# Performance work log

Hardware: AMD Instinct MI355X
Metric: run time of the kernel (lower is better)

The kernel has to match this reference:

```python
import jax, jax.numpy as jnp
import numpy as np

B, N, FIN, H, D = 8, 2048, 64, 4, 32
ALPHA = 0.2  # LeakyReLU negative slope


def setup_inputs() -> dict:
    key = jax.random.key(0)
    k1, k2, k3, k4 = jax.random.split(key, 4)
    h = jax.random.normal(k1, (B, N, FIN), dtype=jnp.float32)
    adj = jax.random.randint(k2, (B, N, N), 0, 2).astype(jnp.int32)
    # ensure self-loops so every softmax row has at least one unmasked entry
    idx = jnp.arange(N)
    adj = adj.at[:, idx, idx].set(1)
    W = jax.random.normal(k3, (FIN, H * D), dtype=jnp.float32) * 0.1
    a = jax.random.normal(k4, (H, 2 * D), dtype=jnp.float32) * 0.1
    return {"h": h, "adj": adj, "W": W, "a": a}


def reference(h, adj, W, a):
    # h: (B,N,Fin), adj: (B,N,N) int, W: (Fin,H*D), a: (H,2D)
    Bn, Nn, _ = h.shape
    Hh, twoD = a.shape
    Dd = twoD // 2
    Wh = (h @ W).reshape(Bn, Nn, Hh, Dd).transpose(0, 2, 1, 3)  # (B,H,N,D)
    # e_ij = leakyrelu(Wh_i . a1 + Wh_j . a2) -- avoids O(N^2 * 2D) concat
    src = jnp.einsum('bhnd,hd->bhn', Wh, a[:, :Dd])  # (B,H,N)
    dst = jnp.einsum('bhnd,hd->bhn', Wh, a[:, Dd:])  # (B,H,N)
    e = jax.nn.leaky_relu(src[:, :, :, None] + dst[:, :, None, :], negative_slope=ALPHA)  # (B,H,N,N)
    e = jnp.where(adj[:, None, :, :] == 0, -jnp.inf, e)
    attn = jax.nn.softmax(e, axis=-1)  # (B,H,N,N)
    out = jnp.einsum('bhij,bhjd->bhid', attn, Wh)  # (B,H,N,D)
    return out.transpose(0, 2, 1, 3).reshape(Bn, Nn, Hh * Dd)
```

## Files before the change

kernel.cpp:

```cpp
#include <hip/hip_runtime.h>

typedef short short8 __attribute__((ext_vector_type(8)));
typedef _Float16 half8 __attribute__((ext_vector_type(8)));
typedef _Float16 half2v __attribute__((ext_vector_type(2)));
typedef float floatx4 __attribute__((ext_vector_type(4)));

extern "C" __device__ _Float16 __ocml_exp2_f16(_Float16);

#define B_   8
#define N_   2048
#define FIN_ 64
#define H_   4
#define D_   32
#define HD_  128
#define JH_  1024
#define ALPHA_ 0.2f
#define LOG2E_ 1.4426950408889634f


__global__ __launch_bounds__(256) void gat_prep4(
    const float* __restrict__ h, const float* __restrict__ W, const float* __restrict__ a,
    unsigned short* __restrict__ WhF, float* __restrict__ src, unsigned short* __restrict__ dstb)
{
    __shared__ float Ws[FIN_][HD_];
    __shared__ float hsT[FIN_][36];
    int bx = blockIdx.x;
    int b = bx >> 6;
    int n0 = (bx & 63) * 32;
    int tid = threadIdx.x;

    #pragma unroll
    for (int it = 0; it < 8; ++it) {
        int idx = it * 256 + tid;
        int k = idx >> 5, c4 = (idx & 31) << 2;
        *(float4*)&Ws[k][c4] = *(const float4*)&W[k * HD_ + c4];
    }
    #pragma unroll
    for (int it = 0; it < 8; ++it) {
        int idx = it * 256 + tid;
        int r = idx >> 6, k = idx & 63;
        hsT[k][r] = h[((size_t)b * N_ + n0 + r) * FIN_ + k];
    }
    __syncthreads();

    int c = tid & 127;
    int rq = tid >> 7;
    int hh = c >> 5, d = c & 31;
    float acc[16];
    #pragma unroll
    for (int r = 0; r < 16; ++r) acc[r] = 0.f;
    for (int k = 0; k < FIN_; ++k) {
        float wv = Ws[k][c];
        float4 h0 = *(const float4*)&hsT[k][rq * 16];
        float4 h1 = *(const float4*)&hsT[k][rq * 16 + 4];
        float4 h2 = *(const float4*)&hsT[k][rq * 16 + 8];
        float4 h3 = *(const float4*)&hsT[k][rq * 16 + 12];
        acc[0]  += h0.x * wv; acc[1]  += h0.y * wv; acc[2]  += h0.z * wv; acc[3]  += h0.w * wv;
        acc[4]  += h1.x * wv; acc[5]  += h1.y * wv; acc[6]  += h1.z * wv; acc[7]  += h1.w * wv;
        acc[8]  += h2.x * wv; acc[9]  += h2.y * wv; acc[10] += h2.z * wv; acc[11] += h2.w * wv;
        acc[12] += h3.x * wv; acc[13] += h3.y * wv; acc[14] += h3.z * wv; acc[15] += h3.w * wv;
    }

    {
        int half = d >> 4, n = d & 15;
        int j0 = n0 + rq * 16;
        int it0 = j0 >> 5;
        int g0 = (j0 >> 3) & 3;
        #pragma unroll
        for (int rr = 0; rr < 2; ++rr) {
            __attribute__((aligned(16))) unsigned pk4[4];
            #pragma unroll
            for (int q = 0; q < 4; ++q)
                pk4[q] = __builtin_bit_cast(unsigned,
                    __builtin_amdgcn_cvt_pkrtz(acc[rr * 8 + 2 * q], acc[rr * 8 + 2 * q + 1]));
            size_t fi = ((((size_t)b * H_ + hh) * 64 + it0) * 2 + half) * 64
                        + (size_t)(g0 + rr) * 16 + n;
            *(uint4*)&WhF[fi * 8] = *(uint4*)pk4;
        }
    }

    float a1v = a[hh * 64 + d];
    float a2v = a[hh * 64 + 32 + d];
    #pragma unroll
    for (int r = 0; r < 16; ++r) {
        float s1 = acc[r] * a1v;
        float s2 = acc[r] * a2v;
        #pragma unroll
        for (int off = 16; off >= 1; off >>= 1) {
            s1 += __shfl_xor(s1, off, 32);
            s2 += __shfl_xor(s2, off, 32);
        }
        if (d == 0) {
            int n = n0 + rq * 16 + r;
            src[(b * H_ + hh) * N_ + n] = s1 * LOG2E_;
            _Float16 hv = (_Float16)(s2 * LOG2E_);
            dstb[(b * H_ + hh) * N_ + n] = __builtin_bit_cast(unsigned short, hv);
        }
    }
}

__global__ __launch_bounds__(256, 4) void gat_main11(
    const int* __restrict__ adj, const unsigned short* __restrict__ WhF,
    const float* __restrict__ src, const unsigned short* __restrict__ dstb,
    float* __restrict__ pO, float* __restrict__ pW)
{
    __shared__ unsigned short dsts[H_ * JH_];
    __shared__ unsigned adjW[16][36];

    int bx = blockIdx.x;
    int b    = bx >> 8;
    int rest = bx & 255;
    int half = rest & 1;
    int i0   = (rest >> 1) * 16;
    int jb   = half * JH_;
    int tid = threadIdx.x;
    int wv = tid >> 6, l = tid & 63;

    #pragma unroll
    for (int it = 0; it < 2; ++it) {
        int idx = it * 256 + tid;
        int hh = idx >> 7, off = (idx & 127) * 8;
        *(uint4*)&dsts[hh * JH_ + off] =
            *(const uint4*)&dstb[(size_t)(b * H_ + hh) * N_ + jb + off];
    }

    const int* adjBase = adj + ((size_t)(b * N_ + i0 + wv * 4)) * N_ + jb + l;

    int vals[16];
    #pragma unroll
    for (int rr = 0; rr < 4; ++rr)
        #pragma unroll
        for (int cc = 0; cc < 4; ++cc)
            vals[rr * 4 + cc] = adjBase[rr * N_ + cc * 64];

    int h = wv, g = l >> 4, m = l & 15;
    int g8 = g << 3;
    _Float16 sv = (_Float16)src[(b * H_ + h) * N_ + i0 + m];
    half2v s2; s2[0] = sv; s2[1] = sv;
    const _Float16 alf = (_Float16)0.2f;
    const unsigned short* WhB =
        WhF + (((size_t)(b * H_ + h) * 64 + half * 32)) * 1024 + l * 8;
    const unsigned short* dstH = &dsts[h * JH_];

    short8 onesS;
    #pragma unroll
    for (int q = 0; q < 8; ++q) onesS[q] = (short)0x3C00;
    half8 ones = __builtin_bit_cast(half8, onesS);

    floatx4 acc0 = {0.f, 0.f, 0.f, 0.f};
    floatx4 acc1 = {0.f, 0.f, 0.f, 0.f};
    floatx4 acc2 = {0.f, 0.f, 0.f, 0.f};

    short8 bf0_c = *(const short8*)&WhB[0];
    short8 bf1_c = *(const short8*)&WhB[512];
    uint4 dv_c;

    for (int q = 0; q < 4; ++q) {
        #pragma unroll
        for (int rr = 0; rr < 4; ++rr)
            #pragma unroll
            for (int cc = 0; cc < 4; ++cc) {
                unsigned long long mk = __ballot(vals[rr * 4 + cc] != 0);
                if (l == 0) {
                    int c = q * 4 + cc;
                    adjW[wv * 4 + rr][2 * c]     = (unsigned)mk;
                    adjW[wv * 4 + rr][2 * c + 1] = (unsigned)(mk >> 32);
                }
            }
        __syncthreads();
        if (q == 0) dv_c = *(const uint4*)&dstH[g8];

        if (q < 3) {
            #pragma unroll
            for (int rr = 0; rr < 4; ++rr)
                #pragma unroll
                for (int cc = 0; cc < 4; ++cc)
                    vals[rr * 4 + cc] = adjBase[rr * N_ + (q + 1) * 256 + cc * 64];
        }

        for (int jj = 0; jj < 8; ++jj) {
            int it = q * 8 + jj;
            int fn = (it + 1) * 1024;
            short8 bf0_n = *(const short8*)&WhB[fn];
            short8 bf1_n = *(const short8*)&WhB[fn + 512];
            int j0n = ((it + 1) << 5) + g8;
            uint4  dv_n  = *(const uint4*)&dstH[(j0n < JH_) ? j0n : g8];

            unsigned sh = adjW[m][it] >> g8;
            const unsigned* du = (const unsigned*)&dv_c;
            __attribute__((aligned(16))) unsigned pk[4];
            #pragma unroll
            for (int c2 = 0; c2 < 4; ++c2) {
                half2v d2 = __builtin_bit_cast(half2v, du[c2]);
                half2v e2 = s2 + d2;
                half2v t2 = e2 * alf;
                e2 = __builtin_elementwise_max(e2, t2);
                half2v x2;
                x2[0] = __ocml_exp2_f16(e2[0]);
                x2[1] = __ocml_exp2_f16(e2[1]);
                unsigned mk = ((((sh >> (2 * c2 + 1)) & 1u) << 16)
                               | ((sh >> (2 * c2)) & 1u)) * 0x3C00u;
                x2 = x2 * __builtin_bit_cast(half2v, mk);
                pk[c2] = __builtin_bit_cast(unsigned, x2);
            }
            half8 af = __builtin_bit_cast(half8, *(uint4*)pk);
            acc0 = __builtin_amdgcn_mfma_f32_16x16x32_f16(
                       af, __builtin_bit_cast(half8, bf0_c), acc0, 0, 0, 0);
            acc1 = __builtin_amdgcn_mfma_f32_16x16x32_f16(
                       af, __builtin_bit_cast(half8, bf1_c), acc1, 0, 0, 0);
            acc2 = __builtin_amdgcn_mfma_f32_16x16x32_f16(af, ones, acc2, 0, 0, 0);
            bf0_c = bf0_n; bf1_c = bf1_n; dv_c = dv_n;
        }
    }

    if (m == 0) {
        #pragma unroll
        for (int r = 0; r < 4; ++r)
            pW[(((size_t)half * B_ + b) * H_ + h) * N_ + i0 + g * 4 + r] = acc2[r];
    }
    #pragma unroll
    for (int r = 0; r < 4; ++r) {
        size_t o = ((size_t)(half * B_ + b) * N_ + i0 + g * 4 + r) * HD_ + h * 32 + m;
        pO[o]      = acc0[r];
        pO[o + 16] = acc1[r];
    }
}

__global__ __launch_bounds__(256) void gat_fin(
    const float* __restrict__ pO, const float* __restrict__ pW, float* __restrict__ out)
{
    int gid = blockIdx.x * 256 + threadIdx.x;
    int c4 = (gid & 31) << 2;
    int i  = (gid >> 5) & (N_ - 1);
    int b  = gid >> 16;
    int hh = c4 >> 5;
    float w0 = pW[((size_t)b * H_ + hh) * N_ + i];
    float w1 = pW[(((size_t)B_ + b) * H_ + hh) * N_ + i];
    float inv = 1.f / (w0 + w1);
    size_t o = ((size_t)b * N_ + i) * HD_ + c4;
    float4 v0 = *(const float4*)&pO[o];
    float4 v1 = *(const float4*)&pO[(size_t)B_ * N_ * HD_ + o];
    float4 r;
    r.x = (v0.x + v1.x) * inv;
    r.y = (v0.y + v1.y) * inv;
    r.z = (v0.z + v1.z) * inv;
    r.w = (v0.w + v1.w) * inv;
    *(float4*)&out[o] = r;
}

extern "C" void kernel_launch(void* const* d_in, const int* in_sizes, int n_in,
                              void* d_out, int out_size, void* d_ws, size_t ws_size,
                              hipStream_t stream) {
    const float* h   = (const float*)d_in[0];
    const int*   adj = (const int*)d_in[1];
    const float* W   = (const float*)d_in[2];
    const float* a   = (const float*)d_in[3];
    float* out = (float*)d_out;

    unsigned short* WhF  = (unsigned short*)d_ws;
    float*          src  = (float*)((char*)d_ws + 4u * 1024 * 1024);
    unsigned short* dstb = (unsigned short*)((char*)d_ws + 4u * 1024 * 1024 + 256u * 1024);
    float*          pO   = (float*)((char*)d_ws + 8u * 1024 * 1024);
    float*          pW   = (float*)((char*)d_ws + 24u * 1024 * 1024);

    gat_prep4<<<B_ * (N_ / 32), 256, 0, stream>>>(h, W, a, WhF, src, dstb);
    gat_main11<<<B_ * (N_ / 16) * 2, 256, 0, stream>>>(adj, WhF, src, dstb, pO, pW);
    gat_fin<<<(B_ * N_ * HD_ / 4) / 256, 256, 0, stream>>>(pO, pW, out);
}
```

Before: 230.7 us.

## Drop the split over neighbour columns and normalize inside the main kernel

Each block now processes all 2048 neighbour columns for its 16 rows instead of half of them. This removes the partial-sum buffers and the separate finalize kernel, so softmax normalization happens directly in registers before the output is written. The change removes one launch and the round trip of partial outputs through global memory. In exchange it halves the grid to 1024 blocks, doubles the serial loop length per block, and doubles the shared-memory footprint for dst values.

Measured after the change: 224.5 us. -2.7%, faster.

```diff
diff --git a/kernel.cpp b/kernel.cpp
--- a/kernel.cpp
+++ b/kernel.cpp
@@ -13,7 +13,6 @@
 #define H_   4
 #define D_   32
 #define HD_  128
-#define JH_  1024
 #define ALPHA_ 0.2f
 #define LOG2E_ 1.4426950408889634f
 
@@ -99,32 +98,29 @@
     }
 }
 
-__global__ __launch_bounds__(256, 4) void gat_main11(
+__global__ __launch_bounds__(256, 4) void gat_main12(
     const int* __restrict__ adj, const unsigned short* __restrict__ WhF,
     const float* __restrict__ src, const unsigned short* __restrict__ dstb,
-    float* __restrict__ pO, float* __restrict__ pW)
+    float* __restrict__ out)
 {
-    __shared__ unsigned short dsts[H_ * JH_];
-    __shared__ unsigned adjW[16][36];
+    __shared__ unsigned short dsts[H_ * N_];
+    __shared__ unsigned adjW[16][68];
 
     int bx = blockIdx.x;
-    int b    = bx >> 8;
-    int rest = bx & 255;
-    int half = rest & 1;
-    int i0   = (rest >> 1) * 16;
-    int jb   = half * JH_;
+    int b  = bx >> 7;
+    int i0 = (bx & 127) * 16;
     int tid = threadIdx.x;
     int wv = tid >> 6, l = tid & 63;
 
     #pragma unroll
-    for (int it = 0; it < 2; ++it) {
+    for (int it = 0; it < 4; ++it) {
         int idx = it * 256 + tid;
-        int hh = idx >> 7, off = (idx & 127) * 8;
-        *(uint4*)&dsts[hh * JH_ + off] =
-            *(const uint4*)&dstb[(size_t)(b * H_ + hh) * N_ + jb + off];
-    }
-
-    const int* adjBase = adj + ((size_t)(b * N_ + i0 + wv * 4)) * N_ + jb + l;
+        int hh = idx >> 8, off = (idx & 255) * 8;
+        *(uint4*)&dsts[hh * N_ + off] =
+            *(const uint4*)&dstb[(size_t)(b * H_ + hh) * N_ + off];
+    }
+
+    const int* adjBase = adj + ((size_t)(b * N_ + i0 + wv * 4)) * N_ + l;
 
     int vals[16];
     #pragma unroll
@@ -139,8 +135,8 @@
     half2v s2; s2[0] = sv; s2[1] = sv;
     const _Float16 alf = (_Float16)0.2f;
     const unsigned short* WhB =
-        WhF + (((size_t)(b * H_ + h) * 64 + half * 32)) * 1024 + l * 8;
-    const unsigned short* dstH = &dsts[h * JH_];
+        WhF + ((size_t)(b * H_ + h) * 64) * 1024 + l * 8;
+    const unsigned short* dstH = &dsts[h * N_];
 
     short8 onesS;
     #pragma unroll
@@ -155,7 +151,7 @@
     short8 bf1_c = *(const short8*)&WhB[512];
     uint4 dv_c;
 
-    for (int q = 0; q < 4; ++q) {
+    for (int q = 0; q < 8; ++q) {
         #pragma unroll
         for (int rr = 0; rr < 4; ++rr)
             #pragma unroll
@@ -170,7 +166,7 @@
         __syncthreads();
         if (q == 0) dv_c = *(const uint4*)&dstH[g8];
 
-        if (q < 3) {
+        if (q < 7) {
             #pragma unroll
             for (int rr = 0; rr < 4; ++rr)
                 #pragma unroll
@@ -184,7 +180,7 @@
             short8 bf0_n = *(const short8*)&WhB[fn];
             short8 bf1_n = *(const short8*)&WhB[fn + 512];
             int j0n = ((it + 1) << 5) + g8;
-            uint4  dv_n  = *(const uint4*)&dstH[(j0n < JH_) ? j0n : g8];
+            uint4  dv_n  = *(const uint4*)&dstH[(j0n < N_) ? j0n : g8];
 
             unsigned sh = adjW[m][it] >> g8;
             const unsigned* du = (const unsigned*)&dv_c;
@@ -213,39 +209,13 @@
         }
     }
 
-    if (m == 0) {
-        #pragma unroll
-        for (int r = 0; r < 4; ++r)
-            pW[(((size_t)half * B_ + b) * H_ + h) * N_ + i0 + g * 4 + r] = acc2[r];
-    }
     #pragma unroll
     for (int r = 0; r < 4; ++r) {
-        size_t o = ((size_t)(half * B_ + b) * N_ + i0 + g * 4 + r) * HD_ + h * 32 + m;
-        pO[o]      = acc0[r];
-        pO[o + 16] = acc1[r];
-    }
-}
-
-__global__ __launch_bounds__(256) void gat_fin(
-    const float* __restrict__ pO, const float* __restrict__ pW, float* __restrict__ out)
-{
-    int gid = blockIdx.x * 256 + threadIdx.x;
-    int c4 = (gid & 31) << 2;
-    int i  = (gid >> 5) & (N_ - 1);
-    int b  = gid >> 16;
-    int hh = c4 >> 5;
-    float w0 = pW[((size_t)b * H_ + hh) * N_ + i];
-    float w1 = pW[(((size_t)B_ + b) * H_ + hh) * N_ + i];
-    float inv = 1.f / (w0 + w1);
-    size_t o = ((size_t)b * N_ + i) * HD_ + c4;
-    float4 v0 = *(const float4*)&pO[o];
-    float4 v1 = *(const float4*)&pO[(size_t)B_ * N_ * HD_ + o];
-    float4 r;
-    r.x = (v0.x + v1.x) * inv;
-    r.y = (v0.y + v1.y) * inv;
-    r.z = (v0.z + v1.z) * inv;
-    r.w = (v0.w + v1.w) * inv;
-    *(float4*)&out[o] = r;
+        float inv = 1.f / acc2[r];
+        size_t o = ((size_t)b * N_ + i0 + g * 4 + r) * HD_ + h * 32 + m;
+        out[o]      = acc0[r] * inv;
+        out[o + 16] = acc1[r] * inv;
+    }
 }
 
 extern "C" void kernel_launch(void* const* d_in, const int* in_sizes, int n_in,
@@ -260,10 +230,7 @@
     unsigned short* WhF  = (unsigned short*)d_ws;
     float*          src  = (float*)((char*)d_ws + 4u * 1024 * 1024);
     unsigned short* dstb = (unsigned short*)((char*)d_ws + 4u * 1024 * 1024 + 256u * 1024);
-    float*          pO   = (float*)((char*)d_ws + 8u * 1024 * 1024);
-    float*          pW   = (float*)((char*)d_ws + 24u * 1024 * 1024);
 
     gat_prep4<<<B_ * (N_ / 32), 256, 0, stream>>>(h, W, a, WhF, src, dstb);
-    gat_main11<<<B_ * (N_ / 16) * 2, 256, 0, stream>>>(adj, WhF, src, dstb, pO, pW);
-    gat_fin<<<(B_ * N_ * HD_ / 4) / 256, 256, 0, stream>>>(pO, pW, out);
+    gat_main12<<<B_ * (N_ / 16), 256, 0, stream>>>(adj, WhF, src, dstb, out);
 }
```

## Deepen WhF prefetch to two stages, vectorize mask reads, raise occupancy hint

Applied to the files above, without the earlier changes.

The main attention kernel now prefetches the WhF B-fragments and dst values two iterations ahead instead of one, using a double register buffer. It also unrolls the inner j loop and reads the adjacency bitmask words with a single vector LDS load per q-chunk. The ballot mask store is combined into one 64-bit write. The launch-bounds occupancy hint goes from 4 to 8 waves. The aim is to hide more global-load latency and cut LDS traffic, but the deeper buffer plus the doubled occupancy target may squeeze registers and cause spills.

After: 281.4 us. +22.0%, slower.

```diff
diff --git a/kernel.cpp b/kernel.cpp
--- a/kernel.cpp
+++ b/kernel.cpp
@@ -99,7 +99,7 @@
     }
 }
 
-__global__ __launch_bounds__(256, 4) void gat_main11(
+__global__ __launch_bounds__(256, 8) void gat_main17(
     const int* __restrict__ adj, const unsigned short* __restrict__ WhF,
     const float* __restrict__ src, const unsigned short* __restrict__ dstb,
     float* __restrict__ pO, float* __restrict__ pW)
@@ -110,9 +110,9 @@
     int bx = blockIdx.x;
     int b    = bx >> 8;
     int rest = bx & 255;
-    int half = rest & 1;
+    int jh   = rest & 1;
     int i0   = (rest >> 1) * 16;
-    int jb   = half * JH_;
+    int jb   = jh * JH_;
     int tid = threadIdx.x;
     int wv = tid >> 6, l = tid & 63;
 
@@ -139,7 +139,7 @@
     half2v s2; s2[0] = sv; s2[1] = sv;
     const _Float16 alf = (_Float16)0.2f;
     const unsigned short* WhB =
-        WhF + (((size_t)(b * H_ + h) * 64 + half * 32)) * 1024 + l * 8;
+        WhF + (((size_t)(b * H_ + h) * 64 + jh * 32)) * 1024 + l * 8;
     const unsigned short* dstH = &dsts[h * JH_];
 
     short8 onesS;
@@ -151,9 +151,11 @@
     floatx4 acc1 = {0.f, 0.f, 0.f, 0.f};
     floatx4 acc2 = {0.f, 0.f, 0.f, 0.f};
 
-    short8 bf0_c = *(const short8*)&WhB[0];
-    short8 bf1_c = *(const short8*)&WhB[512];
-    uint4 dv_c;
+    short8 bf0_a = *(const short8*)&WhB[0];
+    short8 bf1_a = *(const short8*)&WhB[512];
+    short8 bf0_b = *(const short8*)&WhB[1024];
+    short8 bf1_b = *(const short8*)&WhB[1536];
+    uint4 dv_a, dv_b;
 
     for (int q = 0; q < 4; ++q) {
         #pragma unroll
@@ -161,14 +163,17 @@
             #pragma unroll
             for (int cc = 0; cc < 4; ++cc) {
                 unsigned long long mk = __ballot(vals[rr * 4 + cc] != 0);
-                if (l == 0) {
-                    int c = q * 4 + cc;
-                    adjW[wv * 4 + rr][2 * c]     = (unsigned)mk;
-                    adjW[wv * 4 + rr][2 * c + 1] = (unsigned)(mk >> 32);
-                }
+                if (l == 0)
+                    *(unsigned long long*)&adjW[wv * 4 + rr][2 * (q * 4 + cc)] = mk;
             }
         __syncthreads();
-        if (q == 0) dv_c = *(const uint4*)&dstH[g8];
+
+        uint4 shv0 = *(const uint4*)&adjW[m][q * 8];
+        uint4 shv1 = *(const uint4*)&adjW[m][q * 8 + 4];
+        if (q == 0) {
+            dv_a = *(const uint4*)&dstH[g8];
+            dv_b = *(const uint4*)&dstH[32 + g8];
+        }
 
         if (q < 3) {
             #pragma unroll
@@ -178,16 +183,18 @@
                     vals[rr * 4 + cc] = adjBase[rr * N_ + (q + 1) * 256 + cc * 64];
         }
 
+        #pragma unroll
         for (int jj = 0; jj < 8; ++jj) {
             int it = q * 8 + jj;
-            int fn = (it + 1) * 1024;
+            int fn = (it + 2) * 1024;
             short8 bf0_n = *(const short8*)&WhB[fn];
             short8 bf1_n = *(const short8*)&WhB[fn + 512];
-            int j0n = ((it + 1) << 5) + g8;
-            uint4  dv_n  = *(const uint4*)&dstH[(j0n < JH_) ? j0n : g8];
-
-            unsigned sh = adjW[m][it] >> g8;
-            const unsigned* du = (const unsigned*)&dv_c;
+            int j2 = ((it + 2) << 5) + g8;
+            uint4  dv_n = *(const uint4*)&dstH[(j2 < JH_) ? j2 : g8];
+
+            unsigned sh = (jj < 4 ? ((const unsigned*)&shv0)[jj]
+                                  : ((const unsigned*)&shv1)[jj - 4]) >> g8;
+            const unsigned* du = (const unsigned*)&dv_a;
             __attribute__((aligned(16))) unsigned pk[4];
             #pragma unroll
             for (int c2 = 0; c2 < 4; ++c2) {
@@ -205,22 +212,24 @@
             }
             half8 af = __builtin_bit_cast(half8, *(uint4*)pk);
             acc0 = __builtin_amdgcn_mfma_f32_16x16x32_f16(
-                       af, __builtin_bit_cast(half8, bf0_c), acc0, 0, 0, 0);
+                       af, __builtin_bit_cast(half8, bf0_a), acc0, 0, 0, 0);
             acc1 = __builtin_amdgcn_mfma_f32_16x16x32_f16(
-                       af, __builtin_bit_cast(half8, bf1_c), acc1, 0, 0, 0);
+                       af, __builtin_bit_cast(half8, bf1_a), acc1, 0, 0, 0);
             acc2 = __builtin_amdgcn_mfma_f32_16x16x32_f16(af, ones, acc2, 0, 0, 0);
-            bf0_c = bf0_n; bf1_c = bf1_n; dv_c = dv_n;
+            bf0_a = bf0_b; bf0_b = bf0_n;
+            bf1_a = bf1_b; bf1_b = bf1_n;
+            dv_a = dv_b;   dv_b = dv_n;
         }
     }
 
     if (m == 0) {
         #pragma unroll
         for (int r = 0; r < 4; ++r)
-            pW[(((size_t)half * B_ + b) * H_ + h) * N_ + i0 + g * 4 + r] = acc2[r];
+            pW[(((size_t)jh * B_ + b) * H_ + h) * N_ + i0 + g * 4 + r] = acc2[r];
     }
     #pragma unroll
     for (int r = 0; r < 4; ++r) {
-        size_t o = ((size_t)(half * B_ + b) * N_ + i0 + g * 4 + r) * HD_ + h * 32 + m;
+        size_t o = ((size_t)(jh * B_ + b) * N_ + i0 + g * 4 + r) * HD_ + h * 32 + m;
         pO[o]      = acc0[r];
         pO[o + 16] = acc1[r];
     }
@@ -264,6 +273,6 @@
     float*          pW   = (float*)((char*)d_ws + 24u * 1024 * 1024);
 
     gat_prep4<<<B_ * (N_ / 32), 256, 0, stream>>>(h, W, a, WhF, src, dstb);
-    gat_main11<<<B_ * (N_ / 16) * 2, 256, 0, stream>>>(adj, WhF, src, dstb, pO, pW);
+    gat_main17<<<B_ * (N_ / 16) * 2, 256, 0, stream>>>(adj, WhF, src, dstb, pO, pW);
     gat_fin<<<(B_ * N_ * HD_ / 4) / 256, 256, 0, stream>>>(pO, pW, out);
 }
```
